# Kernel tuning notes

Measured on AMD Instinct MI355X. Metric: run time of the kernel, lower is better.

The kernel has to match this reference:

```python
import jax, jax.numpy as jnp
import numpy as np
import math

D_MODEL = 1024
NUM_HEADS = 16
BATCH = 4
SEQ = 2048

def setup_inputs() -> dict:
    key = jax.random.key(0)
    ks = jax.random.split(key, 7)
    s = 1.0 / math.sqrt(D_MODEL)
    return {
        "x": jax.random.normal(ks[0], (BATCH, SEQ, D_MODEL), dtype=jnp.float32),
        "Wq": jax.random.normal(ks[1], (D_MODEL, D_MODEL), dtype=jnp.float32) * s,
        "bq": jax.random.normal(ks[2], (D_MODEL,), dtype=jnp.float32) * s,
        "Wk": jax.random.normal(ks[3], (D_MODEL, D_MODEL), dtype=jnp.float32) * s,
        "bk": jax.random.normal(ks[4], (D_MODEL,), dtype=jnp.float32) * s,
        "Wv": jax.random.normal(ks[5], (D_MODEL, D_MODEL), dtype=jnp.float32) * s,
        "bv": jax.random.normal(ks[6], (D_MODEL,), dtype=jnp.float32) * s,
        "num_heads": NUM_HEADS,
    }

def reference(x, Wq, bq, Wk, bk, Wv, bv, num_heads):
    B, S, D = x.shape
    hd = D // num_heads
    scale = 1.0 / math.sqrt(D)  # NOTE: module scales by sqrt(d_model), not sqrt(head_dim)
    # torch nn.Linear: y = x @ W.T + b
    q = x @ Wq.T + bq
    k = x @ Wk.T + bk
    v = x @ Wv.T + bv
    # Faithful replication of the module's (non-standard) row-major view:
    # (B, S, D) -> (B*H, S, D/H)
    q = q.reshape(B * num_heads, -1, hd)
    k = k.reshape(B * num_heads, -1, hd)
    v = v.reshape(B * num_heads, -1, hd)
    scores = jnp.einsum('bqd,bkd->bqk', q, k) * scale  # [B*H, S, S]
    probs = jax.nn.softmax(scores, axis=-1)
    out = jnp.einsum('bqk,bkd->bqd', probs, v)
    return out.reshape(B, -1, D)
```

## Files before the change

### kernel.cpp

```cpp
#include <hip/hip_runtime.h>
#include <stdint.h>

typedef unsigned short u16;
typedef __attribute__((ext_vector_type(8))) short short8;
typedef __attribute__((ext_vector_type(4))) float f32x4;
typedef __attribute__((ext_vector_type(16))) float f32x16;
typedef __attribute__((ext_vector_type(2))) unsigned int uv2;
typedef __attribute__((ext_vector_type(4))) unsigned int uv4;

#define MFMA16(a, b, c) __builtin_amdgcn_mfma_f32_16x16x32_bf16((a), (b), (c), 0, 0, 0)
#define MFMA32(a, b, c) __builtin_amdgcn_mfma_f32_32x32x16_bf16((a), (b), (c), 0, 0, 0)
#define LOG2E 1.4426950408889634f
#define SCALE 0.03125f
#define KC (SCALE * LOG2E)

__device__ __forceinline__ u16 f2bf(float f) {
  union { float f; uint32_t u; } cv; cv.f = f;
  uint32_t u = cv.u;
  uint32_t r = (u + 0x7fffu + ((u >> 16) & 1u)) >> 16;
  return (u16)r;
}

__device__ __forceinline__ unsigned cvtpk(float lo, float hi) {
  unsigned r;
  asm("v_cvt_pk_bf16_f32 %0, %1, %2" : "=v"(r) : "v"(lo), "v"(hi));
  return r;
}

__device__ __forceinline__ void gld(const void* g, void* l) {
  __builtin_amdgcn_global_load_lds(
      (const __attribute__((address_space(1))) void*)g,
      (__attribute__((address_space(3))) void*)l, 16, 0, 0);
}

__device__ __forceinline__ const short8* tile8(const u16* base, int row, int c) {
  return (const short8*)(base + row * 64 + (((c) ^ (row & 7)) << 3));
}

__global__ void cvt4_kernel(const float* __restrict__ x, const float* __restrict__ wq,
                            const float* __restrict__ wk, const float* __restrict__ wv,
                            u16* __restrict__ xb, u16* __restrict__ wqb,
                            u16* __restrict__ wkb, u16* __restrict__ wvb) {
  const int NX8 = 1048576;
  const int NW8 = 131072;
  const int TOT = NX8 + 3 * NW8;
  int i = blockIdx.x * blockDim.x + threadIdx.x;
  const int stride = gridDim.x * blockDim.x;
  for (; i < TOT; i += stride) {
    const float* src; u16* dst; int j;
    if (i < NX8) { src = x; dst = xb; j = i; }
    else if (i < NX8 + NW8) { src = wq; dst = wqb; j = i - NX8; }
    else if (i < NX8 + 2 * NW8) { src = wk; dst = wkb; j = i - NX8 - NW8; }
    else { src = wv; dst = wvb; j = i - NX8 - 2 * NW8; }
    const f32x4* s = (const f32x4*)src + (size_t)j * 2;
    f32x4 a = s[0], b = s[1];
    short8 o;
    o[0] = (short)f2bf(a[0]); o[1] = (short)f2bf(a[1]);
    o[2] = (short)f2bf(a[2]); o[3] = (short)f2bf(a[3]);
    o[4] = (short)f2bf(b[0]); o[5] = (short)f2bf(b[1]);
    o[6] = (short)f2bf(b[2]); o[7] = (short)f2bf(b[3]);
    *((short8*)dst + j) = o;
  }
}

__global__ __launch_bounds__(256) void gemm_qkv(
    const u16* __restrict__ xb,
    const u16* __restrict__ wqb, const u16* __restrict__ wkb, const u16* __restrict__ wvb,
    const float* __restrict__ bq, const float* __restrict__ bk, const float* __restrict__ bv,
    u16* __restrict__ qo, u16* __restrict__ ko, u16* __restrict__ vo) {
  __shared__ __align__(16) u16 sm[2][128 * 64];

  const int bid = blockIdx.x;
  const int cx = bid & 7, qq = bid >> 3;
  const int m = ((qq & 7) << 3) + cx;
  const int nz = qq >> 3;
  const int n = nz / 3;
  const int z = nz - n * 3;
  const u16* W = (z == 0) ? wqb : (z == 1) ? wkb : wvb;
  const float* bias = (z == 0) ? bq : (z == 1) ? bk : bv;
  u16* out = (z == 0) ? qo : (z == 1) ? ko : vo;
  const float oscale = (z == 0) ? KC : 1.0f;
  const int m0 = m * 128, n0 = n * 128;

  const int t = threadIdx.x;
  const int lane = t & 63;
  const int w = t >> 6;
  const int l15 = lane & 15, l4 = lane >> 4;
  const int mw = (w >> 1) * 64, nw = (w & 1) * 64;

  const int srow8 = lane >> 3;
  const int ssw = ((lane & 7) ^ srow8) << 3;
  const u16* aG = xb + (size_t)(m0 + (w * 4) * 8 + srow8) * 1024 + ssw;
  const u16* bG = W + (size_t)(n0 + (w * 4) * 8 + srow8) * 1024 + ssw;
  u16* aL = &sm[0][0] + (w * 4) * 512 + lane * 8;
  u16* bL = &sm[1][0] + (w * 4) * 512 + lane * 8;

  float biasv[4];
#pragma unroll
  for (int nj = 0; nj < 4; nj++) biasv[nj] = bias[n0 + nw + nj * 16 + l15];

  const f32x4 fz = {0.f, 0.f, 0.f, 0.f};
  f32x4 acc[4][4];
#pragma unroll
  for (int i = 0; i < 4; i++)
#pragma unroll
    for (int j = 0; j < 4; j++) acc[i][j] = fz;

  for (int k0 = 0; k0 < 1024; k0 += 64) {
    __syncthreads();
#pragma unroll
    for (int cc = 0; cc < 4; cc++) {
      gld(aG + k0 + (size_t)cc * 8 * 1024, aL + cc * 512);
      gld(bG + k0 + (size_t)cc * 8 * 1024, bL + cc * 512);
    }
    __syncthreads();
#pragma unroll
    for (int kk = 0; kk < 2; kk++) {
      short8 af[4], bf[4];
#pragma unroll
      for (int mi = 0; mi < 4; mi++) af[mi] = *tile8(&sm[0][0], mw + mi * 16 + l15, kk * 4 + l4);
#pragma unroll
      for (int nj = 0; nj < 4; nj++) bf[nj] = *tile8(&sm[1][0], nw + nj * 16 + l15, kk * 4 + l4);
      __builtin_amdgcn_s_setprio(1);
#pragma unroll
      for (int mi = 0; mi < 4; mi++)
#pragma unroll
        for (int nj = 0; nj < 4; nj++)
          acc[mi][nj] = MFMA16(af[mi], bf[nj], acc[mi][nj]);
      __builtin_amdgcn_s_setprio(0);
    }
  }

  __syncthreads();
  u16* Cs = &sm[0][0] + w * 4096;
#pragma unroll
  for (int mi = 0; mi < 4; mi++)
#pragma unroll
    for (int nj = 0; nj < 4; nj++)
#pragma unroll
      for (int r = 0; r < 4; r++) {
        const int row = mi * 16 + l4 * 4 + r;
        const int col = nj * 16 + l15;
        Cs[row * 64 + (((col >> 3) ^ (row & 7)) << 3) + (col & 7)] =
            f2bf((acc[mi][nj][r] + biasv[nj]) * oscale);
      }
#pragma unroll
  for (int i = 0; i < 8; i++) {
    const int row = i * 8 + (lane >> 3);
    short8 vv = *tile8(Cs, row, lane & 7);
    *(short8*)(out + (size_t)(m0 + mw + row) * 1024 + n0 + nw + (lane & 7) * 8) = vv;
  }
}

__global__ void repack_kv(const u16* __restrict__ k, const u16* __restrict__ v,
                          u16* __restrict__ kpk, u16* __restrict__ vpk) {
  __shared__ __align__(16) u16 LK[4096];
  __shared__ u16 LV[4096];
  const int g = blockIdx.y, tt = blockIdx.x;
  const size_t sb = (size_t)g * 131072 + (size_t)tt * 4096;
  const int t = threadIdx.x;
#pragma unroll
  for (int i = 0; i < 2; i++) {
    const int ccc = t + i * 256;
    const int r = ccc >> 3, d0 = (ccc & 7) * 8;
    short8 dk = *(const short8*)(k + sb + (size_t)r * 64 + d0);
    const int b = r >> 5, ks = d0 >> 4;
    const int L = (r & 31) | (((d0 >> 3) & 1) << 5);
    *(short8*)(LK + ((b * 4 + ks) << 9) + L * 8) = dk;
    short8 dv = *(const short8*)(v + sb + (size_t)r * 64 + d0);
    const int c = r >> 3, j = r & 7;
    const int h2 = d0 >> 5;
    const int base = h2 * 2048 + (c >> 1) * 512 + (c & 1) * 256 + j;
#pragma unroll
    for (int jj = 0; jj < 8; jj++) LV[base + ((d0 & 31) + jj) * 8] = (u16)dv[jj];
  }
  __syncthreads();
#pragma unroll
  for (int i = 0; i < 2; i++) {
    const int ccc = t + i * 256;
    *(short8*)(kpk + sb + ccc * 8) = *(const short8*)(LK + ccc * 8);
    *(short8*)(vpk + sb + ccc * 8) = *(const short8*)(LV + ccc * 8);
  }
}


__device__ __forceinline__ void qblock(f32x16& s, float& lsum, f32x16& o0, f32x16& o1,
                                       const short8* vf) {
  float p[16];
#pragma unroll
  for (int i = 0; i < 16; i++) p[i] = __builtin_amdgcn_exp2f(s[i]);
  float s01 = p[0] + p[1], s23 = p[2] + p[3], s45 = p[4] + p[5], s67 = p[6] + p[7];
  float s89 = p[8] + p[9], sab = p[10] + p[11], scd = p[12] + p[13], sef = p[14] + p[15];
  lsum += ((s01 + s23) + (s45 + s67)) + ((s89 + sab) + (scd + sef));

  short8 pa0, pa1;
  {
    unsigned a0 = cvtpk(p[0], p[1]);
    unsigned a1 = cvtpk(p[2], p[3]);
    unsigned b0 = cvtpk(p[4], p[5]);
    unsigned b1 = cvtpk(p[6], p[7]);
    uv2 r0 = __builtin_amdgcn_permlane32_swap(a0, b0, false, false);
    uv2 r1 = __builtin_amdgcn_permlane32_swap(a1, b1, false, false);
    union { uv4 u; short8 s8; } cc;
    cc.u[0] = r0[0]; cc.u[1] = r1[0]; cc.u[2] = r0[1]; cc.u[3] = r1[1];
    pa0 = cc.s8;
  }
  {
    unsigned a0 = cvtpk(p[8], p[9]);
    unsigned a1 = cvtpk(p[10], p[11]);
    unsigned b0 = cvtpk(p[12], p[13]);
    unsigned b1 = cvtpk(p[14], p[15]);
    uv2 r0 = __builtin_amdgcn_permlane32_swap(a0, b0, false, false);
    uv2 r1 = __builtin_amdgcn_permlane32_swap(a1, b1, false, false);
    union { uv4 u; short8 s8; } cc;
    cc.u[0] = r0[0]; cc.u[1] = r1[0]; cc.u[2] = r0[1]; cc.u[3] = r1[1];
    pa1 = cc.s8;
  }
  o0 = MFMA32(pa0, vf[0], o0);
  o0 = MFMA32(pa1, vf[1], o0);
  o1 = MFMA32(pa0, vf[2], o1);
  o1 = MFMA32(pa1, vf[3], o1);
}

__global__ __launch_bounds__(256, 4) void attn_kernel(const u16* __restrict__ q,
                                                      const u16* __restrict__ kpk,
                                                      const u16* __restrict__ vpk,
                                                      float* __restrict__ out) {
  __shared__ __align__(16) u16 Ks[2][4096];
  const int t = threadIdx.x, lane = t & 63, w = t >> 6;
  const int l31 = lane & 31, hi = lane >> 5;
  const int bid = blockIdx.x;
  const int cx = bid & 7, qq = bid >> 3;
  const int qt = qq & 15;
  const int g = ((qq >> 4) << 3) + cx;
  const size_t gb = (size_t)g * 131072;
  const int q0 = qt * 128 + w * 32;

  const u16* qp = q + gb + (size_t)(q0 + l31) * 64 + hi * 8;
  short8 qf[4];
#pragma unroll
  for (int ks = 0; ks < 4; ks++) qf[ks] = *(const short8*)(qp + ks * 16);

  const u16* kS = kpk + gb + w * 1024 + (size_t)lane * 8;
  const u16* vP = vpk + gb + (size_t)lane * 8;
  const u16* kR0 = &Ks[0][0] + lane * 8;
  const u16* kR1 = &Ks[1][0] + lane * 8;

  f32x16 o0, o1;
#pragma unroll
  for (int i = 0; i < 16; i++) { o0[i] = 0.f; o1[i] = 0.f; }
  float lsum = 0.f;
  f32x16 Z;
#pragma unroll
  for (int i = 0; i < 16; i++) Z[i] = 0.f;

  {
    u16* kD = &Ks[0][0] + w * 1024 + lane * 8;
    gld(kS, kD);
    gld(kS + 512, kD + 512);
  }
  __syncthreads();

  for (int tt = 0; tt < 32; ++tt) {
    const int cur = tt & 1;
    if (tt < 31) {
      u16* kD = (cur ? &Ks[0][0] : &Ks[1][0]) + w * 1024 + lane * 8;
      const u16* kSn = kS + (size_t)(tt + 1) * 4096;
      gld(kSn, kD);
      gld(kSn + 512, kD + 512);
    }
    const u16* kR = cur ? kR1 : kR0;
    const u16* vT = vP + (size_t)tt * 4096;
#pragma unroll
    for (int b = 0; b < 2; b++) {
      short8 vf[4];
      vf[0] = *(const short8*)(vT + (b << 1) * 512);
      vf[1] = *(const short8*)(vT + ((b << 1) | 1) * 512);
      vf[2] = *(const short8*)(vT + 2048 + (b << 1) * 512);
      vf[3] = *(const short8*)(vT + 2048 + ((b << 1) | 1) * 512);
      short8 kf[4];
#pragma unroll
      for (int ks = 0; ks < 4; ks++)
        kf[ks] = *(const short8*)(kR + ((b << 2) | ks) * 512);
      f32x16 s = MFMA32(kf[0], qf[0], Z);
      s = MFMA32(kf[1], qf[1], s);
      s = MFMA32(kf[2], qf[2], s);
      s = MFMA32(kf[3], qf[3], s);
      qblock(s, lsum, o0, o1, vf);
    }
    __syncthreads();
  }

  float lt = lsum + __shfl_xor(lsum, 32);
  float inv = 1.0f / lt;
  float* ob = out + gb + (size_t)q0 * 64;
#pragma unroll
  for (int r = 0; r < 16; r++) {
    int qr = (r & 3) + 8 * (r >> 2) + 4 * hi;
    float ir = __shfl(inv, qr);
    ob[(size_t)qr * 64 + l31] = o0[r] * ir;
    ob[(size_t)qr * 64 + 32 + l31] = o1[r] * ir;
  }
}

extern "C" void kernel_launch(void* const* d_in, const int* in_sizes, int n_in,
                              void* d_out, int out_size, void* d_ws, size_t ws_size,
                              hipStream_t stream) {
  const float* x  = (const float*)d_in[0];
  const float* Wq = (const float*)d_in[1];
  const float* bq = (const float*)d_in[2];
  const float* Wk = (const float*)d_in[3];
  const float* bk = (const float*)d_in[4];
  const float* Wv = (const float*)d_in[5];
  const float* bv = (const float*)d_in[6];
  float* out = (float*)d_out;

  const size_t NX = 8388608;
  const size_t NW = 1048576;
  u16* ws = (u16*)d_ws;
  u16* xb  = ws;
  u16* wqb = xb + NX;
  u16* wkb = wqb + NW;
  u16* wvb = wkb + NW;
  u16* qb  = wvb + NW;
  u16* kb  = qb + NX;
  u16* vb  = kb + NX;
  u16* vpk = vb + NX;
  u16* kpk = xb;

  cvt4_kernel<<<2048, 256, 0, stream>>>(x, Wq, Wk, Wv, xb, wqb, wkb, wvb);

  gemm_qkv<<<1536, 256, 0, stream>>>(xb, wqb, wkb, wvb, bq, bk, bv, qb, kb, vb);

  repack_kv<<<dim3(32, 64), 256, 0, stream>>>(kb, vb, kpk, vpk);

  attn_kernel<<<1024, 256, 0, stream>>>(qb, kpk, vpk, out);
}
```

Before: 156.8 us.

## Process two query tiles per wave and load K directly to registers

Each wave now handles 64 query rows (two 32-row tiles) instead of 32, so each K/V fragment loaded is reused for two QK and PV products. The LDS staging buffer and per-iteration block barriers are removed; K and V fragments are loaded straight from global memory into registers with a software double buffer. The grid is halved and launch bounds lowered to 2 blocks per SM to make room for the doubled accumulators. Register pressure and lower occupancy may limit latency hiding, and K now comes from global or L2 rather than LDS.

```diff
diff --git a/kernel.cpp b/kernel.cpp
--- a/kernel.cpp
+++ b/kernel.cpp
@@ -222,84 +222,96 @@
   o1 = MFMA32(pa1, vf[3], o1);
 }
 
-__global__ __launch_bounds__(256, 4) void attn_kernel(const u16* __restrict__ q,
+#define LOADK(KF, P) do {                         \
+    KF[0] = *(const short8*)((P));                \
+    KF[1] = *(const short8*)((P) + 512);          \
+    KF[2] = *(const short8*)((P) + 1024);         \
+    KF[3] = *(const short8*)((P) + 1536);         \
+  } while (0)
+#define LOADV0(VF, P) do {                        \
+    VF[0] = *(const short8*)((P));                \
+    VF[1] = *(const short8*)((P) + 512);          \
+    VF[2] = *(const short8*)((P) + 2048);         \
+    VF[3] = *(const short8*)((P) + 2560);         \
+  } while (0)
+#define LOADV1(VF, P) do {                        \
+    VF[0] = *(const short8*)((P) + 1024);         \
+    VF[1] = *(const short8*)((P) + 1536);         \
+    VF[2] = *(const short8*)((P) + 3072);         \
+    VF[3] = *(const short8*)((P) + 3584);         \
+  } while (0)
+#define QKQB(KF, QF, LS, OA, OB, VF) do {         \
+    f32x16 s_ = MFMA32(KF[0], QF[0], Z);          \
+    s_ = MFMA32(KF[1], QF[1], s_);                \
+    s_ = MFMA32(KF[2], QF[2], s_);                \
+    s_ = MFMA32(KF[3], QF[3], s_);                \
+    qblock(s_, LS, OA, OB, VF);                   \
+  } while (0)
+
+__global__ __launch_bounds__(256, 2) void attn_kernel(const u16* __restrict__ q,
                                                       const u16* __restrict__ kpk,
                                                       const u16* __restrict__ vpk,
                                                       float* __restrict__ out) {
-  __shared__ __align__(16) u16 Ks[2][4096];
   const int t = threadIdx.x, lane = t & 63, w = t >> 6;
   const int l31 = lane & 31, hi = lane >> 5;
   const int bid = blockIdx.x;
   const int cx = bid & 7, qq = bid >> 3;
-  const int qt = qq & 15;
-  const int g = ((qq >> 4) << 3) + cx;
+  const int qt = qq & 7;
+  const int g = ((qq >> 3) << 3) + cx;
   const size_t gb = (size_t)g * 131072;
-  const int q0 = qt * 128 + w * 32;
+  const int q0 = qt * 256 + w * 64;
 
   const u16* qp = q + gb + (size_t)(q0 + l31) * 64 + hi * 8;
-  short8 qf[4];
-#pragma unroll
-  for (int ks = 0; ks < 4; ks++) qf[ks] = *(const short8*)(qp + ks * 16);
-
-  const u16* kS = kpk + gb + w * 1024 + (size_t)lane * 8;
+  short8 qfA[4], qfB[4];
+#pragma unroll
+  for (int ks = 0; ks < 4; ks++) {
+    qfA[ks] = *(const short8*)(qp + ks * 16);
+    qfB[ks] = *(const short8*)(qp + 32 * 64 + ks * 16);
+  }
+
+  const u16* kP = kpk + gb + (size_t)lane * 8;
   const u16* vP = vpk + gb + (size_t)lane * 8;
-  const u16* kR0 = &Ks[0][0] + lane * 8;
-  const u16* kR1 = &Ks[1][0] + lane * 8;
-
-  f32x16 o0, o1;
-#pragma unroll
-  for (int i = 0; i < 16; i++) { o0[i] = 0.f; o1[i] = 0.f; }
-  float lsum = 0.f;
+
+  f32x16 oA0, oA1, oB0, oB1;
+#pragma unroll
+  for (int i = 0; i < 16; i++) { oA0[i] = 0.f; oA1[i] = 0.f; oB0[i] = 0.f; oB1[i] = 0.f; }
+  float lA = 0.f, lB = 0.f;
   f32x16 Z;
 #pragma unroll
   for (int i = 0; i < 16; i++) Z[i] = 0.f;
 
-  {
-    u16* kD = &Ks[0][0] + w * 1024 + lane * 8;
-    gld(kS, kD);
-    gld(kS + 512, kD + 512);
-  }
-  __syncthreads();
+  short8 kfA[4], kfB[4], vfA[4], vfB[4];
+  LOADK(kfA, kP);
+  LOADV0(vfA, vP);
 
   for (int tt = 0; tt < 32; ++tt) {
-    const int cur = tt & 1;
+    LOADK(kfB, kP + 2048);
+    LOADV1(vfB, vP);
+    QKQB(kfA, qfA, lA, oA0, oA1, vfA);
+    QKQB(kfA, qfB, lB, oB0, oB1, vfA);
+    kP += 4096; vP += 4096;
     if (tt < 31) {
-      u16* kD = (cur ? &Ks[0][0] : &Ks[1][0]) + w * 1024 + lane * 8;
-      const u16* kSn = kS + (size_t)(tt + 1) * 4096;
-      gld(kSn, kD);
-      gld(kSn + 512, kD + 512);
+      LOADK(kfA, kP);
+      LOADV0(vfA, vP);
     }
-    const u16* kR = cur ? kR1 : kR0;
-    const u16* vT = vP + (size_t)tt * 4096;
-#pragma unroll
-    for (int b = 0; b < 2; b++) {
-      short8 vf[4];
-      vf[0] = *(const short8*)(vT + (b << 1) * 512);
-      vf[1] = *(const short8*)(vT + ((b << 1) | 1) * 512);
-      vf[2] = *(const short8*)(vT + 2048 + (b << 1) * 512);
-      vf[3] = *(const short8*)(vT + 2048 + ((b << 1) | 1) * 512);
-      short8 kf[4];
-#pragma unroll
-      for (int ks = 0; ks < 4; ks++)
-        kf[ks] = *(const short8*)(kR + ((b << 2) | ks) * 512);
-      f32x16 s = MFMA32(kf[0], qf[0], Z);
-      s = MFMA32(kf[1], qf[1], s);
-      s = MFMA32(kf[2], qf[2], s);
-      s = MFMA32(kf[3], qf[3], s);
-      qblock(s, lsum, o0, o1, vf);
-    }
-    __syncthreads();
-  }
-
-  float lt = lsum + __shfl_xor(lsum, 32);
-  float inv = 1.0f / lt;
-  float* ob = out + gb + (size_t)q0 * 64;
+    QKQB(kfB, qfA, lA, oA0, oA1, vfB);
+    QKQB(kfB, qfB, lB, oB0, oB1, vfB);
+  }
+
+  float ltA = lA + __shfl_xor(lA, 32);
+  float ltB = lB + __shfl_xor(lB, 32);
+  float invA = 1.0f / ltA, invB = 1.0f / ltB;
+  float* obA = out + gb + (size_t)q0 * 64;
+  float* obB = obA + 32 * 64;
 #pragma unroll
   for (int r = 0; r < 16; r++) {
     int qr = (r & 3) + 8 * (r >> 2) + 4 * hi;
-    float ir = __shfl(inv, qr);
-    ob[(size_t)qr * 64 + l31] = o0[r] * ir;
-    ob[(size_t)qr * 64 + 32 + l31] = o1[r] * ir;
+    float irA = __shfl(invA, qr);
+    float irB = __shfl(invB, qr);
+    obA[(size_t)qr * 64 + l31] = oA0[r] * irA;
+    obA[(size_t)qr * 64 + 32 + l31] = oA1[r] * irA;
+    obB[(size_t)qr * 64 + l31] = oB0[r] * irB;
+    obB[(size_t)qr * 64 + 32 + l31] = oB1[r] * irB;
   }
 }
 
@@ -334,5 +346,5 @@
 
   repack_kv<<<dim3(32, 64), 256, 0, stream>>>(kb, vb, kpk, vpk);
 
-  attn_kernel<<<1024, 256, 0, stream>>>(qb, kpk, vpk, out);
-}
+  attn_kernel<<<512, 256, 0, stream>>>(qb, kpk, vpk, out);
+}
```

Result: faster. 153.4 us, median of 3 (-2.1%).
